# Kernel tuning notes

Hardware: AMD Instinct MI355X
Metric: run time of the kernel (lower is better)

## Reference

```python
import jax, jax.numpy as jnp
import numpy as np

B, S, D_IN, D_OUT, H = 4, 2048, 1024, 1024, 16
HD = D_OUT // H


def setup_inputs() -> dict:
    key = jax.random.key(0)
    ks = jax.random.split(key, 6)
    sc_in = 1.0 / np.sqrt(D_IN)
    sc_out = 1.0 / np.sqrt(D_OUT)
    return {
        "x": jax.random.normal(ks[0], (B, S, D_IN), dtype=jnp.float32),
        "Wq": jax.random.normal(ks[1], (D_IN, D_OUT), dtype=jnp.float32) * sc_in,
        "Wk": jax.random.normal(ks[2], (D_IN, D_OUT), dtype=jnp.float32) * sc_in,
        "Wv": jax.random.normal(ks[3], (D_IN, D_OUT), dtype=jnp.float32) * sc_in,
        "Wo": jax.random.normal(ks[4], (D_OUT, D_OUT), dtype=jnp.float32) * sc_out,
        "bo": jax.random.normal(ks[5], (D_OUT,), dtype=jnp.float32) * 0.01,
    }


def reference(x, Wq, Wk, Wv, Wo, bo):
    b, s, _ = x.shape
    # projections -> [b, h, s, hd]
    def split_heads(t):
        return t.reshape(b, s, H, HD).transpose(0, 2, 1, 3)
    q = split_heads(x @ Wq)
    k = split_heads(x @ Wk)
    v = split_heads(x @ Wv)
    # full score matrix [b, h, s, s], causal mask, scaled softmax
    scores = jnp.einsum("bhqd,bhkd->bhqk", q, k)
    causal = jnp.tril(jnp.ones((s, s), dtype=bool))
    scores = jnp.where(causal, scores, -jnp.inf)
    attn = jax.nn.softmax(scores / np.sqrt(HD), axis=-1)
    # dropout p=0.0 -> identity
    ctx = jnp.einsum("bhqk,bhkd->bhqd", attn, v)
    ctx = ctx.transpose(0, 2, 1, 3).reshape(b, s, D_OUT)
    return ctx @ Wo + bo
```

## Files before the change

kernel.cpp:

```cpp
#include <hip/hip_runtime.h>


typedef float  f32x4  __attribute__((ext_vector_type(4)));
typedef __bf16 bf16x8 __attribute__((ext_vector_type(8)));
typedef __bf16 bf16x4 __attribute__((ext_vector_type(4)));

#define AS(n) __attribute__((address_space(n)))

__device__ __forceinline__ void gload16(const void* g, void* l) {
    __builtin_amdgcn_global_load_lds((const AS(1) void*)g, (AS(3) void*)l, 16, 0, 0);
}

__device__ __forceinline__ f32x4 mfma16(bf16x8 a, bf16x8 b, f32x4 c) {
    return __builtin_amdgcn_mfma_f32_16x16x32_bf16(a, b, c, 0, 0, 0);
}

__global__ void convert_x_kernel(const float4* __restrict__ x, __bf16* __restrict__ xb) {
    int t = blockIdx.x * 256 + threadIdx.x;
    float4 v = x[t];
    bf16x4 o = { (__bf16)v.x, (__bf16)v.y, (__bf16)v.z, (__bf16)v.w };
    ((bf16x4*)xb)[t] = o;
}

__global__ void transpose_w_kernel(const float* __restrict__ Wq, const float* __restrict__ Wk,
                                   const float* __restrict__ Wv, const float* __restrict__ Wo,
                                   __bf16* __restrict__ wqkvt, __bf16* __restrict__ wot) {
    const float* src; __bf16* dst;
    int z = blockIdx.z;
    if (z == 0)      { src = Wq; dst = wqkvt; }
    else if (z == 1) { src = Wk; dst = wqkvt + 1048576; }
    else if (z == 2) { src = Wv; dst = wqkvt + 2097152; }
    else             { src = Wo; dst = wot; }
    __shared__ float tile[32][33];
    int tx = threadIdx.x, ty = threadIdx.y;
    int x = blockIdx.x * 32 + tx;
    int y0 = blockIdx.y * 32;
#pragma unroll
    for (int i = ty; i < 32; i += 8) tile[i][tx] = src[(size_t)(y0 + i) * 1024 + x];
    __syncthreads();
    int xo = blockIdx.y * 32 + tx;
    int yo0 = blockIdx.x * 32;
#pragma unroll
    for (int i = ty; i < 32; i += 8) dst[(size_t)(yo0 + i) * 1024 + xo] = (__bf16)tile[tx][i];
}

__global__ __launch_bounds__(256, 2) void gemm_qkv_kernel(
        const __bf16* __restrict__ A, const __bf16* __restrict__ Bt,
        __bf16* __restrict__ Qp, __bf16* __restrict__ Kp, __bf16* __restrict__ Vp) {
    __shared__ __bf16 lA[128 * 32];
    __shared__ __bf16 lB[128 * 32];
    int tid = threadIdx.x;
    int m0 = blockIdx.x * 128, n0 = blockIdx.y * 128;
    int w = tid >> 6, lane = tid & 63, quad = lane >> 4, l15 = lane & 15;
    int wm = (w & 1) * 64, wn = (w >> 1) * 64;
    f32x4 acc[4][4] = {};
    int rowS = tid >> 2, kc = tid & 3;
    const __bf16* Abase = A + (size_t)m0 * 1024;
    const __bf16* Bbase = Bt + (size_t)n0 * 1024;
    for (int kt = 0; kt < 32; kt++) {
        int k0 = kt * 32;
        gload16(Abase + (size_t)rowS * 1024 + k0 + kc * 8,        &lA[tid * 8]);
        gload16(Abase + (size_t)(rowS + 64) * 1024 + k0 + kc * 8, &lA[(tid + 256) * 8]);
        gload16(Bbase + (size_t)rowS * 1024 + k0 + kc * 8,        &lB[tid * 8]);
        gload16(Bbase + (size_t)(rowS + 64) * 1024 + k0 + kc * 8, &lB[(tid + 256) * 8]);
        __syncthreads();
        bf16x8 a[4], b[4];
#pragma unroll
        for (int i = 0; i < 4; i++) a[i] = *(const bf16x8*)&lA[(wm + i * 16 + l15) * 32 + quad * 8];
#pragma unroll
        for (int j = 0; j < 4; j++) b[j] = *(const bf16x8*)&lB[(wn + j * 16 + l15) * 32 + quad * 8];
#pragma unroll
        for (int i = 0; i < 4; i++)
#pragma unroll
            for (int j = 0; j < 4; j++)
                acc[i][j] = mfma16(a[i], b[j], acc[i][j]);
        __syncthreads();
    }
    int mat = n0 >> 10;
    int ncol0 = n0 & 1023;
    __bf16* dst = (mat == 0) ? Qp : ((mat == 1) ? Kp : Vp);
    float sc = (mat == 0) ? 0.1803368801111204f : 1.0f;
#pragma unroll
    for (int i = 0; i < 4; i++) {
#pragma unroll
        for (int j = 0; j < 4; j++) {
            int n = ncol0 + wn + j * 16 + l15;
            int h = n >> 6, d = n & 63;
#pragma unroll
            for (int r = 0; r < 4; r++) {
                int m = m0 + wm + i * 16 + quad * 4 + r;
                int bb = m >> 11, s = m & 2047;
                dst[((((size_t)bb * 16 + h) * 2048 + s) << 6) + d] = (__bf16)(acc[i][j][r] * sc);
            }
        }
    }
}

__global__ void transpose_v_kernel(const __bf16* __restrict__ Vp, __bf16* __restrict__ Vt) {
    int st = blockIdx.x;
    int bh = blockIdx.y;
    __shared__ __bf16 t[64 * 72];
    int tid = threadIdx.x;
    const __bf16* src = Vp + (((size_t)bh * 2048) + st * 64) * 64;
    int s = tid >> 2, c = tid & 3;
    *(bf16x8*)&t[s * 72 + c * 16]     = *(const bf16x8*)(src + s * 64 + c * 16);
    *(bf16x8*)&t[s * 72 + c * 16 + 8] = *(const bf16x8*)(src + s * 64 + c * 16 + 8);
    __syncthreads();
    int d = tid >> 2, c2 = tid & 3;
    bf16x8 o1, o2;
#pragma unroll
    for (int e = 0; e < 8; e++) o1[e] = t[(c2 * 16 + e) * 72 + d];
#pragma unroll
    for (int e = 0; e < 8; e++) o2[e] = t[(c2 * 16 + 8 + e) * 72 + d];
    __bf16* dst = Vt + (((size_t)bh * 64) + d) * 2048 + st * 64 + c2 * 16;
    *(bf16x8*)dst = o1;
    *(bf16x8*)(dst + 8) = o2;
}

__global__ __launch_bounds__(256, 2) void attn_kernel(
        const __bf16* __restrict__ Q, const __bf16* __restrict__ K,
        const __bf16* __restrict__ Vt, __bf16* __restrict__ ctx) {
    int xb = blockIdx.x;
    int bh = blockIdx.y;
    int b = bh >> 4, h = bh & 15;
    const __bf16* Qb = Q  + (size_t)bh * (2048 * 64);
    const __bf16* Kb = K  + (size_t)bh * (2048 * 64);
    const __bf16* Vb = Vt + (size_t)bh * (64 * 2048);
    __shared__ __bf16 sK[2][64 * 72];
    __shared__ __bf16 sV[2][64 * 72];
    __shared__ __bf16 sP[128 * 72];
    int tid = threadIdx.x, w = tid >> 6, lane = tid & 63, quad = lane >> 4, l15 = lane & 15;
    int srow = tid >> 2, scol = tid & 3;
    int vd = tid >> 2, vc = tid & 3;
    const bf16x8 vone = { (__bf16)1.0f, (__bf16)1.0f, (__bf16)1.0f, (__bf16)1.0f,
                          (__bf16)1.0f, (__bf16)1.0f, (__bf16)1.0f, (__bf16)1.0f };

    for (int half = 0; half < 2; half++) {
        int qt = half ? (15 - xb) : xb;
        int q0 = qt * 128;
        int nkt = 2 * qt + 2;
        bf16x8 aQ[2][2];
#pragma unroll
        for (int h2 = 0; h2 < 2; h2++)
#pragma unroll
            for (int c = 0; c < 2; c++)
                aQ[h2][c] = *(const bf16x8*)(Qb + (size_t)(q0 + w * 32 + h2 * 16 + l15) * 64 + c * 32 + quad * 8);
        f32x4 o[2][4] = {};
        f32x4 lac[2] = {};
        if (half) __syncthreads();
        {
            const __bf16* kp = Kb + srow * 64 + scol * 16;
            const __bf16* vp = Vb + (size_t)vd * 2048 + vc * 16;
            bf16x8 kA = *(const bf16x8*)kp;
            bf16x8 kB = *(const bf16x8*)(kp + 8);
            bf16x8 vA = *(const bf16x8*)vp;
            bf16x8 vB = *(const bf16x8*)(vp + 8);
            *(bf16x8*)&sK[0][srow * 72 + scol * 16]     = kA;
            *(bf16x8*)&sK[0][srow * 72 + scol * 16 + 8] = kB;
            *(bf16x8*)&sV[0][vd * 72 + vc * 16]         = vA;
            *(bf16x8*)&sV[0][vd * 72 + vc * 16 + 8]     = vB;
        }
        for (int kt = 0; kt < nkt; kt++) {
            int cur = kt & 1;
            __syncthreads();
            bf16x8 kA, kB, vA, vB;
            if (kt + 1 < nkt) {
                const __bf16* kp = Kb + ((kt + 1) * 64 + srow) * 64 + scol * 16;
                const __bf16* vp = Vb + (size_t)vd * 2048 + (kt + 1) * 64 + vc * 16;
                kA = *(const bf16x8*)kp;  kB = *(const bf16x8*)(kp + 8);
                vA = *(const bf16x8*)vp;  vB = *(const bf16x8*)(vp + 8);
            }
            int mb = kt * 64 - q0;
            bool diag = (kt >= 2 * qt);
            if (!(diag && (mb - w * 32 >= 32))) {
                f32x4 s[2][4] = {};
#pragma unroll
                for (int c = 0; c < 2; c++)
#pragma unroll
                    for (int j = 0; j < 4; j++) {
                        bf16x8 kf = *(const bf16x8*)&sK[cur][(j * 16 + l15) * 72 + c * 32 + quad * 8];
                        s[0][j] = mfma16(aQ[0][c], kf, s[0][j]);
                        s[1][j] = mfma16(aQ[1][c], kf, s[1][j]);
                    }
                if (diag && (mb + 63 > w * 32)) {
#pragma unroll
                    for (int h2 = 0; h2 < 2; h2++)
#pragma unroll
                        for (int j = 0; j < 4; j++) {
                            int key = j * 16 + l15 + mb;
#pragma unroll
                            for (int r = 0; r < 4; r++)
                                if (key > w * 32 + h2 * 16 + quad * 4 + r) s[h2][j][r] = -1e30f;
                        }
                }
#pragma unroll
                for (int h2 = 0; h2 < 2; h2++)
#pragma unroll
                    for (int j = 0; j < 4; j++)
#pragma unroll
                        for (int r = 0; r < 4; r++)
                            s[h2][j][r] = exp2f(s[h2][j][r]);
#pragma unroll
                for (int h2 = 0; h2 < 2; h2++)
#pragma unroll
                    for (int j = 0; j < 4; j++) {
                        int kg = ((j ^ quad) << 4) + l15;
#pragma unroll
                        for (int r = 0; r < 4; r++)
                            sP[(w * 32 + h2 * 16 + quad * 4 + r) * 72 + kg] = (__bf16)s[h2][j][r];
                    }
                int pswz = (l15 >> 2) << 4;
#pragma unroll
                for (int h2 = 0; h2 < 2; h2++) {
                    int prow = (w * 32 + h2 * 16 + l15) * 72;
                    bf16x8 p0 = *(const bf16x8*)&sP[prow + ((quad * 8) ^ pswz)];
                    bf16x8 p1 = *(const bf16x8*)&sP[prow + ((quad * 8 + 32) ^ pswz)];
                    lac[h2] = mfma16(p0, vone, lac[h2]);
                    lac[h2] = mfma16(p1, vone, lac[h2]);
#pragma unroll
                    for (int dj = 0; dj < 4; dj++) {
                        int vrow = (dj * 16 + l15) * 72;
                        bf16x8 v0 = *(const bf16x8*)&sV[cur][vrow + quad * 8];
                        bf16x8 v1 = *(const bf16x8*)&sV[cur][vrow + quad * 8 + 32];
                        f32x4 t = mfma16(p0, v0, o[h2][dj]);
                        o[h2][dj] = mfma16(p1, v1, t);
                    }
                }
            }
            if (kt + 1 < nkt) {
                *(bf16x8*)&sK[1 - cur][srow * 72 + scol * 16]     = kA;
                *(bf16x8*)&sK[1 - cur][srow * 72 + scol * 16 + 8] = kB;
                *(bf16x8*)&sV[1 - cur][vd * 72 + vc * 16]         = vA;
                *(bf16x8*)&sV[1 - cur][vd * 72 + vc * 16 + 8]     = vB;
            }
        }
#pragma unroll
        for (int h2 = 0; h2 < 2; h2++)
#pragma unroll
            for (int r = 0; r < 4; r++) {
                float inv = 1.0f / lac[h2][r];
                int q = q0 + w * 32 + h2 * 16 + quad * 4 + r;
                size_t base = (((size_t)b * 2048 + q) << 10) + h * 64;
#pragma unroll
                for (int dj = 0; dj < 4; dj++)
                    ctx[base + dj * 16 + l15] = (__bf16)(o[h2][dj][r] * inv);
            }
    }
}

__global__ __launch_bounds__(256, 2) void gemm_out_kernel(
        const __bf16* __restrict__ A, const __bf16* __restrict__ Bt,
        const float* __restrict__ bo, float* __restrict__ out) {
    __shared__ __bf16 lA[128 * 32];
    __shared__ __bf16 lB[128 * 32];
    int tid = threadIdx.x;
    int m0 = blockIdx.x * 128, n0 = blockIdx.y * 128;
    int w = tid >> 6, lane = tid & 63, quad = lane >> 4, l15 = lane & 15;
    int wm = (w & 1) * 64, wn = (w >> 1) * 64;
    f32x4 acc[4][4] = {};
    int rowS = tid >> 2, kc = tid & 3;
    const __bf16* Abase = A + (size_t)m0 * 1024;
    const __bf16* Bbase = Bt + (size_t)n0 * 1024;
    for (int kt = 0; kt < 32; kt++) {
        int k0 = kt * 32;
        gload16(Abase + (size_t)rowS * 1024 + k0 + kc * 8,        &lA[tid * 8]);
        gload16(Abase + (size_t)(rowS + 64) * 1024 + k0 + kc * 8, &lA[(tid + 256) * 8]);
        gload16(Bbase + (size_t)rowS * 1024 + k0 + kc * 8,        &lB[tid * 8]);
        gload16(Bbase + (size_t)(rowS + 64) * 1024 + k0 + kc * 8, &lB[(tid + 256) * 8]);
        __syncthreads();
        bf16x8 a[4], b[4];
#pragma unroll
        for (int i = 0; i < 4; i++) a[i] = *(const bf16x8*)&lA[(wm + i * 16 + l15) * 32 + quad * 8];
#pragma unroll
        for (int j = 0; j < 4; j++) b[j] = *(const bf16x8*)&lB[(wn + j * 16 + l15) * 32 + quad * 8];
#pragma unroll
        for (int i = 0; i < 4; i++)
#pragma unroll
            for (int j = 0; j < 4; j++)
                acc[i][j] = mfma16(a[i], b[j], acc[i][j]);
        __syncthreads();
    }
#pragma unroll
    for (int j = 0; j < 4; j++) {
        int n = n0 + wn + j * 16 + l15;
        float bias = bo[n];
#pragma unroll
        for (int i = 0; i < 4; i++)
#pragma unroll
            for (int r = 0; r < 4; r++) {
                int m = m0 + wm + i * 16 + quad * 4 + r;
                out[(size_t)m * 1024 + n] = acc[i][j][r] + bias;
            }
    }
}

extern "C" void kernel_launch(void* const* d_in, const int* in_sizes, int n_in,
                              void* d_out, int out_size, void* d_ws, size_t ws_size,
                              hipStream_t stream) {
    const float* x  = (const float*)d_in[0];
    const float* Wq = (const float*)d_in[1];
    const float* Wk = (const float*)d_in[2];
    const float* Wv = (const float*)d_in[3];
    const float* Wo = (const float*)d_in[4];
    const float* bo = (const float*)d_in[5];
    float* out = (float*)d_out;

    __bf16* ws    = (__bf16*)d_ws;
    __bf16* xb    = ws;
    __bf16* wqkvt = xb + 8388608;
    __bf16* wot   = wqkvt + 3145728;
    __bf16* Qp    = wot + 1048576;
    __bf16* Kp    = Qp + 8388608;
    __bf16* Vp    = Kp + 8388608;
    __bf16* ctx   = Vp + 8388608;
    __bf16* Vt    = xb;

    convert_x_kernel<<<8192, 256, 0, stream>>>((const float4*)x, xb);
    transpose_w_kernel<<<dim3(32, 32, 4), dim3(32, 8), 0, stream>>>(Wq, Wk, Wv, Wo, wqkvt, wot);
    gemm_qkv_kernel<<<dim3(64, 24), 256, 0, stream>>>(xb, wqkvt, Qp, Kp, Vp);
    transpose_v_kernel<<<dim3(32, 64), 256, 0, stream>>>(Vp, Vt);
    attn_kernel<<<dim3(8, 64), 256, 0, stream>>>(Qp, Kp, Vt, ctx);
    gemm_out_kernel<<<dim3(64, 8), 256, 0, stream>>>(ctx, wot, bo, out);
}
```

Before: 272.4 us.

## Fuse prep kernels, write V transposed from QKV GEMM, add MFMA priority hints

Merges the x conversion and weight transposes into one launch. The QKV GEMM epilogue now writes V directly in transposed layout through a shared-memory tile, which removes the separate transpose_v kernel and its extra round trip through global memory. In the attention kernel, V fragments are preloaded into registers before the PV MFMAs, and s_setprio raises wave priority around the MFMA blocks. The trade-off is a large extra LDS buffer in the GEMM (about 34 KB), which may reduce occupancy.

```diff
diff --git a/kernel.cpp b/kernel.cpp
--- a/kernel.cpp
+++ b/kernel.cpp
@@ -15,40 +15,45 @@
     return __builtin_amdgcn_mfma_f32_16x16x32_bf16(a, b, c, 0, 0, 0);
 }
 
-__global__ void convert_x_kernel(const float4* __restrict__ x, __bf16* __restrict__ xb) {
-    int t = blockIdx.x * 256 + threadIdx.x;
-    float4 v = x[t];
-    bf16x4 o = { (__bf16)v.x, (__bf16)v.y, (__bf16)v.z, (__bf16)v.w };
-    ((bf16x4*)xb)[t] = o;
-}
-
-__global__ void transpose_w_kernel(const float* __restrict__ Wq, const float* __restrict__ Wk,
-                                   const float* __restrict__ Wv, const float* __restrict__ Wo,
-                                   __bf16* __restrict__ wqkvt, __bf16* __restrict__ wot) {
+__global__ void prep_kernel(const float4* __restrict__ x, __bf16* __restrict__ xb,
+                            const float* __restrict__ Wq, const float* __restrict__ Wk,
+                            const float* __restrict__ Wv, const float* __restrict__ Wo,
+                            __bf16* __restrict__ wqkvt, __bf16* __restrict__ wot) {
+    __shared__ float tile[32][33];
+    int bid = blockIdx.x, tid = threadIdx.x;
+    if (bid < 8192) {
+        int t = bid * 256 + tid;
+        float4 v = x[t];
+        bf16x4 o = { (__bf16)v.x, (__bf16)v.y, (__bf16)v.z, (__bf16)v.w };
+        ((bf16x4*)xb)[t] = o;
+        return;
+    }
+    int idx = bid - 8192;
+    int z = idx >> 10, rest = idx & 1023;
+    int by = rest >> 5, bx = rest & 31;
     const float* src; __bf16* dst;
-    int z = blockIdx.z;
     if (z == 0)      { src = Wq; dst = wqkvt; }
     else if (z == 1) { src = Wk; dst = wqkvt + 1048576; }
     else if (z == 2) { src = Wv; dst = wqkvt + 2097152; }
     else             { src = Wo; dst = wot; }
-    __shared__ float tile[32][33];
-    int tx = threadIdx.x, ty = threadIdx.y;
-    int x = blockIdx.x * 32 + tx;
-    int y0 = blockIdx.y * 32;
-#pragma unroll
-    for (int i = ty; i < 32; i += 8) tile[i][tx] = src[(size_t)(y0 + i) * 1024 + x];
+    int tx = tid & 31, ty = tid >> 5;
+    int xcol = bx * 32 + tx;
+    int y0 = by * 32;
+#pragma unroll
+    for (int i = ty; i < 32; i += 8) tile[i][tx] = src[(size_t)(y0 + i) * 1024 + xcol];
     __syncthreads();
-    int xo = blockIdx.y * 32 + tx;
-    int yo0 = blockIdx.x * 32;
+    int xo = by * 32 + tx;
+    int yo0 = bx * 32;
 #pragma unroll
     for (int i = ty; i < 32; i += 8) dst[(size_t)(yo0 + i) * 1024 + xo] = (__bf16)tile[tx][i];
 }
 
 __global__ __launch_bounds__(256, 2) void gemm_qkv_kernel(
         const __bf16* __restrict__ A, const __bf16* __restrict__ Bt,
-        __bf16* __restrict__ Qp, __bf16* __restrict__ Kp, __bf16* __restrict__ Vp) {
+        __bf16* __restrict__ Qp, __bf16* __restrict__ Kp, __bf16* __restrict__ Vt) {
     __shared__ __bf16 lA[128 * 32];
     __shared__ __bf16 lB[128 * 32];
+    __shared__ __bf16 lT[128 * 136];
     int tid = threadIdx.x;
     int m0 = blockIdx.x * 128, n0 = blockIdx.y * 128;
     int w = tid >> 6, lane = tid & 63, quad = lane >> 4, l15 = lane & 15;
@@ -78,43 +83,41 @@
     }
     int mat = n0 >> 10;
     int ncol0 = n0 & 1023;
-    __bf16* dst = (mat == 0) ? Qp : ((mat == 1) ? Kp : Vp);
-    float sc = (mat == 0) ? 0.1803368801111204f : 1.0f;
-#pragma unroll
-    for (int i = 0; i < 4; i++) {
-#pragma unroll
-        for (int j = 0; j < 4; j++) {
-            int n = ncol0 + wn + j * 16 + l15;
-            int h = n >> 6, d = n & 63;
-#pragma unroll
-            for (int r = 0; r < 4; r++) {
-                int m = m0 + wm + i * 16 + quad * 4 + r;
-                int bb = m >> 11, s = m & 2047;
-                dst[((((size_t)bb * 16 + h) * 2048 + s) << 6) + d] = (__bf16)(acc[i][j][r] * sc);
+    if (mat < 2) {
+        __bf16* dst = (mat == 0) ? Qp : Kp;
+        float sc = (mat == 0) ? 0.1803368801111204f : 1.0f;
+#pragma unroll
+        for (int i = 0; i < 4; i++) {
+#pragma unroll
+            for (int j = 0; j < 4; j++) {
+                int n = ncol0 + wn + j * 16 + l15;
+                int h = n >> 6, d = n & 63;
+#pragma unroll
+                for (int r = 0; r < 4; r++) {
+                    int m = m0 + wm + i * 16 + quad * 4 + r;
+                    int bb = m >> 11, s = m & 2047;
+                    dst[((((size_t)bb * 16 + h) * 2048 + s) << 6) + d] = (__bf16)(acc[i][j][r] * sc);
+                }
             }
         }
-    }
-}
-
-__global__ void transpose_v_kernel(const __bf16* __restrict__ Vp, __bf16* __restrict__ Vt) {
-    int st = blockIdx.x;
-    int bh = blockIdx.y;
-    __shared__ __bf16 t[64 * 72];
-    int tid = threadIdx.x;
-    const __bf16* src = Vp + (((size_t)bh * 2048) + st * 64) * 64;
-    int s = tid >> 2, c = tid & 3;
-    *(bf16x8*)&t[s * 72 + c * 16]     = *(const bf16x8*)(src + s * 64 + c * 16);
-    *(bf16x8*)&t[s * 72 + c * 16 + 8] = *(const bf16x8*)(src + s * 64 + c * 16 + 8);
-    __syncthreads();
-    int d = tid >> 2, c2 = tid & 3;
-    bf16x8 o1, o2;
-#pragma unroll
-    for (int e = 0; e < 8; e++) o1[e] = t[(c2 * 16 + e) * 72 + d];
-#pragma unroll
-    for (int e = 0; e < 8; e++) o2[e] = t[(c2 * 16 + 8 + e) * 72 + d];
-    __bf16* dst = Vt + (((size_t)bh * 64) + d) * 2048 + st * 64 + c2 * 16;
-    *(bf16x8*)dst = o1;
-    *(bf16x8*)(dst + 8) = o2;
+    } else {
+#pragma unroll
+        for (int i = 0; i < 4; i++)
+#pragma unroll
+            for (int j = 0; j < 4; j++)
+#pragma unroll
+                for (int r = 0; r < 4; r++)
+                    lT[(wn + j * 16 + l15) * 136 + wm + i * 16 + quad * 4 + r] = (__bf16)acc[i][j][r];
+        __syncthreads();
+        int row = tid >> 1, c0 = (tid & 1) * 64;
+        int n = ncol0 + row;
+        int hh = n >> 6, d = n & 63;
+        int bb = m0 >> 11, s0 = (m0 & 2047) + c0;
+        __bf16* dst = Vt + (((size_t)(bb * 16 + hh)) * 64 + d) * 2048 + s0;
+#pragma unroll
+        for (int e = 0; e < 8; e++)
+            *(bf16x8*)(dst + e * 8) = *(const bf16x8*)&lT[row * 136 + c0 + e * 8];
+    }
 }
 
 __global__ __launch_bounds__(256, 2) void attn_kernel(
@@ -174,6 +177,7 @@
             bool diag = (kt >= 2 * qt);
             if (!(diag && (mb - w * 32 >= 32))) {
                 f32x4 s[2][4] = {};
+                __builtin_amdgcn_s_setprio(1);
 #pragma unroll
                 for (int c = 0; c < 2; c++)
 #pragma unroll
@@ -182,6 +186,7 @@
                         s[0][j] = mfma16(aQ[0][c], kf, s[0][j]);
                         s[1][j] = mfma16(aQ[1][c], kf, s[1][j]);
                     }
+                __builtin_amdgcn_s_setprio(0);
                 if (diag && (mb + 63 > w * 32)) {
 #pragma unroll
                     for (int h2 = 0; h2 < 2; h2++)
@@ -209,7 +214,15 @@
                         for (int r = 0; r < 4; r++)
                             sP[(w * 32 + h2 * 16 + quad * 4 + r) * 72 + kg] = (__bf16)s[h2][j][r];
                     }
+                bf16x8 vv0[4], vv1[4];
+#pragma unroll
+                for (int dj = 0; dj < 4; dj++) {
+                    int vrow = (dj * 16 + l15) * 72;
+                    vv0[dj] = *(const bf16x8*)&sV[cur][vrow + quad * 8];
+                    vv1[dj] = *(const bf16x8*)&sV[cur][vrow + quad * 8 + 32];
+                }
                 int pswz = (l15 >> 2) << 4;
+                __builtin_amdgcn_s_setprio(1);
 #pragma unroll
                 for (int h2 = 0; h2 < 2; h2++) {
                     int prow = (w * 32 + h2 * 16 + l15) * 72;
@@ -219,13 +232,11 @@
                     lac[h2] = mfma16(p1, vone, lac[h2]);
 #pragma unroll
                     for (int dj = 0; dj < 4; dj++) {
-                        int vrow = (dj * 16 + l15) * 72;
-                        bf16x8 v0 = *(const bf16x8*)&sV[cur][vrow + quad * 8];
-                        bf16x8 v1 = *(const bf16x8*)&sV[cur][vrow + quad * 8 + 32];
-                        f32x4 t = mfma16(p0, v0, o[h2][dj]);
-                        o[h2][dj] = mfma16(p1, v1, t);
+                        f32x4 t = mfma16(p0, vv0[dj], o[h2][dj]);
+                        o[h2][dj] = mfma16(p1, vv1[dj], t);
                     }
                 }
+                __builtin_amdgcn_s_setprio(0);
             }
             if (kt + 1 < nkt) {
                 *(bf16x8*)&sK[1 - cur][srow * 72 + scol * 16]     = kA;
@@ -311,14 +322,11 @@
     __bf16* wot   = wqkvt + 3145728;
     __bf16* Qp    = wot + 1048576;
     __bf16* Kp    = Qp + 8388608;
-    __bf16* Vp    = Kp + 8388608;
-    __bf16* ctx   = Vp + 8388608;
-    __bf16* Vt    = xb;
-
-    convert_x_kernel<<<8192, 256, 0, stream>>>((const float4*)x, xb);
-    transpose_w_kernel<<<dim3(32, 32, 4), dim3(32, 8), 0, stream>>>(Wq, Wk, Wv, Wo, wqkvt, wot);
-    gemm_qkv_kernel<<<dim3(64, 24), 256, 0, stream>>>(xb, wqkvt, Qp, Kp, Vp);
-    transpose_v_kernel<<<dim3(32, 64), 256, 0, stream>>>(Vp, Vt);
+    __bf16* Vt    = Kp + 8388608;
+    __bf16* ctx   = Vt + 8388608;
+
+    prep_kernel<<<12288, 256, 0, stream>>>((const float4*)x, xb, Wq, Wk, Wv, Wo, wqkvt, wot);
+    gemm_qkv_kernel<<<dim3(64, 24), 256, 0, stream>>>(xb, wqkvt, Qp, Kp, Vt);
     attn_kernel<<<dim3(8, 64), 256, 0, stream>>>(Qp, Kp, Vt, ctx);
     gemm_out_kernel<<<dim3(64, 8), 256, 0, stream>>>(ctx, wot, bo, out);
 }
```

Measured after the change: 262.7 us. 3.6% less time.
